# Optimization experiments

Hardware: AMD Instinct MI355X
Metric: run time of the kernel (lower is better)

## Reference

```python
import jax, jax.numpy as jnp
import numpy as np

NEG = -9.0e15

def gat_layer(X, adj_mask, W, Wb, a1, a2, ab):
    # X: [N, Fin]; W: [Fin, Fout]; a1,a2: [Fout]; ab: scalar
    h = X @ W + Wb                                   # [N, Fout]
    # a([h_i || h_j]) = h_i@a1 + h_j@a2 + ab  (decomposition of concat+linear)
    e = jax.nn.leaky_relu((h @ a1)[:, None] + (h @ a2)[None, :] + ab,
                          negative_slope=0.2)        # [N, N]
    e = jnp.where(adj_mask, e, NEG)
    attn = jax.nn.softmax(e, axis=1)                 # [N, N]
    return jax.nn.elu(attn @ h)                      # [N, Fout]

def setup_inputs() -> dict:
    key = jax.random.key(0)
    ks = jax.random.split(key, 12)
    N, Fin, Fh, H, Fout = 4096, 512, 128, 4, 64
    X = jax.random.normal(ks[0], (N, Fin), dtype=jnp.float32)
    adjacency_matrix = jax.random.randint(ks[1], (N, N), 0, 2, dtype=jnp.int32)
    s_in = 1.0 / np.sqrt(Fin)
    s_a = 1.0 / np.sqrt(2 * Fh)
    W_h  = jax.random.uniform(ks[2], (H, Fin, Fh), jnp.float32, -s_in, s_in)
    b_h  = jax.random.uniform(ks[3], (H, Fh), jnp.float32, -s_in, s_in)
    a1_h = jax.random.uniform(ks[4], (H, Fh), jnp.float32, -s_a, s_a)
    a2_h = jax.random.uniform(ks[5], (H, Fh), jnp.float32, -s_a, s_a)
    ab_h = jax.random.uniform(ks[6], (H,), jnp.float32, -s_a, s_a)
    Fcat = H * Fh
    s_c = 1.0 / np.sqrt(Fcat)
    s_ao = 1.0 / np.sqrt(2 * Fout)
    W_o  = jax.random.uniform(ks[7], (Fcat, Fout), jnp.float32, -s_c, s_c)
    b_o  = jax.random.uniform(ks[8], (Fout,), jnp.float32, -s_c, s_c)
    a1_o = jax.random.uniform(ks[9], (Fout,), jnp.float32, -s_ao, s_ao)
    a2_o = jax.random.uniform(ks[10], (Fout,), jnp.float32, -s_ao, s_ao)
    ab_o = jax.random.uniform(ks[11], (), jnp.float32, -s_ao, s_ao)
    return {"X": X, "adjacency_matrix": adjacency_matrix,
            "W_h": W_h, "b_h": b_h, "a1_h": a1_h, "a2_h": a2_h, "ab_h": ab_h,
            "W_o": W_o, "b_o": b_o, "a1_o": a1_o, "a2_o": a2_o, "ab_o": ab_o}

def reference(X, adjacency_matrix, W_h, b_h, a1_h, a2_h, ab_h,
              W_o, b_o, a1_o, a2_o, ab_o):
    adj_mask = adjacency_matrix > 0
    # per-head attention layers, vmapped over heads
    heads = jax.vmap(gat_layer, in_axes=(None, None, 0, 0, 0, 0, 0))(
        X, adj_mask, W_h, b_h, a1_h, a2_h, ab_h)      # [H, N, Fh]
    H, N, Fh = heads.shape
    x = jnp.transpose(heads, (1, 0, 2)).reshape(N, H * Fh)  # concat along features
    x = gat_layer(x, adj_mask, W_o, b_o, a1_o, a2_o, ab_o)  # [N, Fout]
    return jax.nn.log_softmax(x, axis=1)
```

## Files before the change

### kernel.cpp

```cpp
#include <hip/hip_runtime.h>
#include <math.h>

#define NN 4096
#define LOG2E 1.44269504088896340736f

using f32x2  = __attribute__((ext_vector_type(2))) float;
using f32x4  = __attribute__((ext_vector_type(4))) float;
using bf16x4 = __attribute__((ext_vector_type(4))) __bf16;
using bf16x8 = __attribute__((ext_vector_type(8))) __bf16;

#if __has_builtin(__builtin_amdgcn_exp2f)
#define EXP2(x) __builtin_amdgcn_exp2f(x)
#else
#define EXP2(x) __expf((x) * 0.6931471805599453f)
#endif

__device__ __forceinline__ void barrier_lgkm() {
    asm volatile("s_waitcnt lgkmcnt(0)\ns_barrier" ::: "memory");
}

template<int FH>
__device__ __forceinline__ void stage_tile(const __bf16* __restrict__ hgp,
                                           __bf16* dst, int tid) {
#pragma unroll
    for (int it = 0; it < FH / 32; it++) {
        int c = tid + it * 256;
        int f = c >> 3, sl = c & 7;
        int g = sl ^ (f & 7);
        __builtin_amdgcn_global_load_lds(
            (const __attribute__((address_space(1))) void*)(hgp + (size_t)f * NN + g * 8),
            (__attribute__((address_space(3))) void*)(dst + (size_t)c * 8), 16, 0, 0);
    }
}

__device__ __forceinline__ void stage_g(const __bf16* __restrict__ base, int ldk,
                                        __bf16* dst, int tid) {
#pragma unroll
    for (int it = 0; it < 2; it++) {
        int c = tid + it * 256;
        int f = c >> 3, sl = c & 7;
        int g = sl ^ (f & 7);
        __builtin_amdgcn_global_load_lds(
            (const __attribute__((address_space(1))) void*)(base + (size_t)f * ldk + g * 8),
            (__attribute__((address_space(3))) void*)(dst + (size_t)c * 8), 16, 0, 0);
    }
}

__global__ void pack_adj_kernel(const int* __restrict__ adj,
                                unsigned long long* __restrict__ bits) {
    int gw = (blockIdx.x * blockDim.x + threadIdx.x) >> 6;
    int lane = threadIdx.x & 63;
    int v = adj[(size_t)gw * 64 + lane];
    unsigned long long m = __ballot(v > 0);
    if (lane == 0) bits[gw] = m;
}

__global__ void prepack_kernel(const float* __restrict__ W_h, const float* __restrict__ b_h,
                               const float* __restrict__ W_o,
                               __bf16* __restrict__ Bt1, float* __restrict__ biasp,
                               __bf16* __restrict__ Bt2) {
    int idx = blockIdx.x * 256 + threadIdx.x;
    {
        int n = idx >> 9, k = idx & 511;
        int h = n >> 7, f = n & 127;
        Bt1[idx] = (__bf16)W_h[(size_t)h * 512 * 128 + k * 128 + f];
    }
    if (idx < 64 * 512) {
        int n = idx >> 9, k = idx & 511;
        Bt2[idx] = (__bf16)W_o[k * 64 + n];
    }
    if (idx < 512) biasp[idx] = b_h[idx];
}

__global__ void cast_bf16_kernel(const float* __restrict__ src, __bf16* __restrict__ dst) {
    int i = blockIdx.x * 256 + threadIdx.x;
    f32x4 v = *(const f32x4*)(src + (size_t)i * 4);
    bf16x4 o;
#pragma unroll
    for (int q = 0; q < 4; q++) o[q] = (__bf16)v[q];
    *(bf16x4*)(dst + (size_t)i * 4) = o;
}

__global__ __launch_bounds__(256) void gemm_fused_kernel(
    const __bf16* __restrict__ A, const __bf16* __restrict__ Bt,
    const float* __restrict__ bias,
    const float* __restrict__ a1, const float* __restrict__ a2,
    __bf16* __restrict__ Ht, float* __restrict__ s1, float* __restrict__ s2,
    int M, int N, int K)
{
    __shared__ __attribute__((aligned(16))) __bf16 As[2][64 * 64];
    __shared__ __attribute__((aligned(16))) __bf16 Bs[2][64 * 64];
    const int tid = threadIdx.x, w = tid >> 6, l = tid & 63, o = l >> 4, rl = l & 15;
    const int bm = blockIdx.y * 64, bn = blockIdx.x * 64;
    f32x4 acc[4] = {};
    stage_g(A + (size_t)bm * K, K, &As[0][0], tid);
    stage_g(Bt + (size_t)bn * K, K, &Bs[0][0], tid);
    const int KB = K / 64;
    for (int kb = 0; kb < KB; kb++) {
        int b = kb & 1;
        __syncthreads();
        if (kb + 1 < KB) {
            stage_g(A + (size_t)bm * K + (kb + 1) * 64, K, &As[b ^ 1][0], tid);
            stage_g(Bt + (size_t)bn * K + (kb + 1) * 64, K, &Bs[b ^ 1][0], tid);
        }
#pragma unroll
        for (int kt = 0; kt < 2; kt++) {
            int ra = w * 16 + rl;
            int cg = kt * 4 + o;
            bf16x8 af = *(const bf16x8*)(&As[b][(ra * 8 + (cg ^ (ra & 7))) * 8]);
#pragma unroll
            for (int nt = 0; nt < 4; nt++) {
                int rb = nt * 16 + rl;
                bf16x8 bfr = *(const bf16x8*)(&Bs[b][(rb * 8 + (cg ^ (rb & 7))) * 8]);
                acc[nt] = __builtin_amdgcn_mfma_f32_16x16x32_bf16(af, bfr, acc[nt], 0, 0, 0);
            }
        }
    }
    const int head = bn >> 7;
    const int row_base = bm + w * 16 + o * 4;
    float p1[4] = {0.f, 0.f, 0.f, 0.f}, p2[4] = {0.f, 0.f, 0.f, 0.f};
#pragma unroll
    for (int nt = 0; nt < 4; nt++) {
        int col = bn + nt * 16 + rl;
        float bv = bias[col];
        float a1v = a1[col] * LOG2E, a2v = a2[col] * LOG2E;
        bf16x4 hv;
#pragma unroll
        for (int r4 = 0; r4 < 4; r4++) {
            float h = acc[nt][r4] + bv;
            hv[r4] = (__bf16)h;
            p1[r4] += h * a1v;
            p2[r4] += h * a2v;
        }
        *(bf16x4*)(Ht + (size_t)col * M + row_base) = hv;
    }
#pragma unroll
    for (int r4 = 0; r4 < 4; r4++)
#pragma unroll
        for (int off = 1; off < 16; off <<= 1) {
            p1[r4] += __shfl_xor(p1[r4], off, 64);
            p2[r4] += __shfl_xor(p2[r4], off, 64);
        }
    if (rl == 0)
#pragma unroll
        for (int r4 = 0; r4 < 4; r4++) {
            atomicAdd(&s1[(size_t)head * M + row_base + r4], p1[r4]);
            atomicAdd(&s2[(size_t)head * M + row_base + r4], p2[r4]);
        }
}

__global__ void smax_kernel(const float* __restrict__ s2, float* __restrict__ s2max) {
    const float* p = s2 + (size_t)blockIdx.x * NN;
    int t = threadIdx.x;
    float m = -INFINITY;
    for (int i = t; i < NN; i += 256) m = fmaxf(m, p[i]);
#pragma unroll
    for (int off = 1; off < 64; off <<= 1) m = fmaxf(m, __shfl_xor(m, off, 64));
    __shared__ float red[4];
    if ((t & 63) == 0) red[t >> 6] = m;
    __syncthreads();
    if (t == 0) s2max[blockIdx.x] = fmaxf(fmaxf(red[0], red[1]), fmaxf(red[2], red[3]));
}

template<int FH, int JSPLIT>
__global__ __launch_bounds__(256, 4) void attn_kernel(
    const __bf16* __restrict__ Htg,
    const unsigned long long* __restrict__ adj_bits,
    const float* __restrict__ s1_all, const float* __restrict__ s2_all,
    const float* __restrict__ s2max_all, const float* __restrict__ ab_all,
    __bf16* __restrict__ accp,
    float* __restrict__ lg,
    int ldo)
{
    constexpr int NJT = NN / 64 / JSPLIT;
    constexpr int NTW = FH / 64;
    const int head = blockIdx.y;
    const int js   = blockIdx.z;
    const int row0 = blockIdx.x * 64;
    const int jt0  = js * NJT;
    const int tid = threadIdx.x;
    const int w = tid >> 6, l = tid & 63, o = l >> 4, rl = l & 15;
    const int myrow = row0 + w * 16 + rl;

    __shared__ __attribute__((aligned(16))) __bf16 hbuf[2][FH * 64];
    __shared__ __attribute__((aligned(16))) __bf16 plds[8 * 64 * 8];

    const float* s2 = s2_all + (size_t)head * NN;
    const __bf16* hg = Htg + (size_t)head * FH * NN;
    const float s1r = s1_all[(size_t)head * NN + myrow] + ab_all[head] * LOG2E;
    float mrow; { float x = s1r + s2max_all[head]; mrow = fmaxf(x, 0.2f * x); }
    const float u0 = s1r - mrow;
    const float v0 = fmaf(0.2f, s1r, -mrow);
    float lacc = 0.f;
    f32x4 acc[4][NTW] = {};

    unsigned long long aw;
    f32x4 sA0, sB0, sA1, sB1;
    bf16x8 fc0, fc1;
    bf16x8 fn0, fn1;

    auto PLOAD = [&](int jt) {
        aw = adj_bits[(size_t)myrow * 64 + jt];
        const float* sp = s2 + jt * 64 + o * 8;
        sA0 = *(const f32x4*)(sp);       sB0 = *(const f32x4*)(sp + 4);
        sA1 = *(const f32x4*)(sp + 32);  sB1 = *(const f32x4*)(sp + 36);
    };
    auto PMATH = [&](bf16x8& f0, bf16x8& f1) {
        float ps = 0.f;
        {
            unsigned int mb = (unsigned int)(aw >> (o * 8)) & 0xFFu;
#pragma unroll
            for (int q = 0; q < 8; q++) {
                float s = (q < 4) ? sA0[q] : sB0[q - 4];
                float t = fmaxf(s + u0, fmaf(0.2f, s, v0));
                t = ((mb >> q) & 1u) ? t : -1.0e20f;
                float p = EXP2(t);
                f0[q] = (__bf16)p; ps += p;
            }
        }
        {
            unsigned int mb = (unsigned int)(aw >> (32 + o * 8)) & 0xFFu;
#pragma unroll
            for (int q = 0; q < 8; q++) {
                float s = (q < 4) ? sA1[q] : sB1[q - 4];
                float t = fmaxf(s + u0, fmaf(0.2f, s, v0));
                t = ((mb >> q) & 1u) ? t : -1.0e20f;
                float p = EXP2(t);
                f1[q] = (__bf16)p; ps += p;
            }
        }
        lacc += ps;
    };

    stage_tile<FH>(hg + (size_t)jt0 * 64, &hbuf[0][0], tid);
    PLOAD(jt0);
    PMATH(fc0, fc1);
    PLOAD(jt0 + 1);

    for (int jl = 0; jl < NJT; jl++) {
        const int b = jl & 1;
        const int jt = jt0 + jl;
        *(bf16x8*)(&plds[((w * 2 + 0) * 64 + l) * 8]) = fc0;
        *(bf16x8*)(&plds[((w * 2 + 1) * 64 + l) * 8]) = fc1;
        __syncthreads();
        if (jl + 1 < NJT) {
            stage_tile<FH>(hg + (size_t)(jt + 1) * 64, &hbuf[b ^ 1][0], tid);
            PMATH(fn0, fn1);
        }
        if (jl + 2 < NJT) PLOAD(jt + 2);
        __builtin_amdgcn_s_setprio(1);
#pragma unroll
        for (int kt = 0; kt < 2; kt++) {
            bf16x8 b0, b1;
            {
                int f = (w * NTW + 0) * 16 + rl;
                int slot = (kt * 4 + o) ^ (rl & 7);
                b0 = *(const bf16x8*)(&hbuf[b][(f * 8 + slot) * 8]);
            }
            if constexpr (NTW > 1) {
                int f = (w * NTW + 1) * 16 + rl;
                int slot = (kt * 4 + o) ^ (rl & 7);
                b1 = *(const bf16x8*)(&hbuf[b][(f * 8 + slot) * 8]);
            }
#pragma unroll
            for (int mt = 0; mt < 4; mt++) {
                bf16x8 af = (mt == w) ? (kt ? fc1 : fc0)
                          : *(const bf16x8*)(&plds[((mt * 2 + kt) * 64 + l) * 8]);
                acc[mt][0] = __builtin_amdgcn_mfma_f32_16x16x32_bf16(
                    af, b0, acc[mt][0], 0, 0, 0);
                if constexpr (NTW > 1)
                    acc[mt][1] = __builtin_amdgcn_mfma_f32_16x16x32_bf16(
                        af, b1, acc[mt][1], 0, 0, 0);
            }
        }
        __builtin_amdgcn_s_setprio(0);
        barrier_lgkm();
        fc0 = fn0; fc1 = fn1;
    }
    lacc += __shfl_xor(lacc, 16, 64);
    lacc += __shfl_xor(lacc, 32, 64);
    if (l < 16) lg[((size_t)head * JSPLIT + js) * NN + row0 + w * 16 + l] = lacc;
#pragma unroll
    for (int mt = 0; mt < 4; mt++)
#pragma unroll
        for (int ntl = 0; ntl < NTW; ntl++)
#pragma unroll
            for (int r4 = 0; r4 < 4; r4++) {
                int grow = row0 + mt * 16 + o * 4 + r4;
                int gcol = head * FH + (w * NTW + ntl) * 16 + rl;
                accp[((size_t)js * NN + grow) * ldo + gcol] = (__bf16)acc[mt][ntl][r4];
            }
}

__global__ void combine1_kernel(const __bf16* __restrict__ accp, const float* __restrict__ lg,
                                __bf16* __restrict__ outb) {
    int gid = blockIdx.x * 256 + threadIdx.x;
    int row = gid >> 7, c4 = (gid & 127) * 4;
    int head = c4 >> 7;
    float lsum = 0.f;
#pragma unroll
    for (int js = 0; js < 4; js++) lsum += lg[((size_t)head * 4 + js) * NN + row];
    float inv = lsum > 0.f ? 1.f / lsum : 0.f;
    float v[4] = {0.f, 0.f, 0.f, 0.f};
#pragma unroll
    for (int js = 0; js < 4; js++) {
        bf16x4 t = *(const bf16x4*)(accp + ((size_t)js * NN + row) * 512 + c4);
#pragma unroll
        for (int q = 0; q < 4; q++) v[q] += (float)t[q];
    }
    bf16x4 ob;
#pragma unroll
    for (int q = 0; q < 4; q++) {
        float x = v[q] * inv;
        x = x > 0.f ? x : __expf(x) - 1.f;
        ob[q] = (__bf16)x;
    }
    *(bf16x4*)(outb + (size_t)row * 512 + c4) = ob;
}

__global__ void combine2_kernel(const __bf16* __restrict__ accp, const float* __restrict__ lg,
                                float* __restrict__ out) {
    int row = (blockIdx.x * 256 + threadIdx.x) >> 6;
    int lane = threadIdx.x & 63;
    if (row >= NN) return;
    float lsum = 0.f, v = 0.f;
#pragma unroll
    for (int js = 0; js < 16; js++) {
        lsum += lg[(size_t)js * NN + row];
        v += (float)accp[((size_t)js * NN + row) * 64 + lane];
    }
    float inv = lsum > 0.f ? 1.f / lsum : 0.f;
    v *= inv;
    v = v > 0.f ? v : __expf(v) - 1.f;
    float m = v;
#pragma unroll
    for (int off = 1; off < 64; off <<= 1) m = fmaxf(m, __shfl_xor(m, off, 64));
    float ex = __expf(v - m);
    float s = ex;
#pragma unroll
    for (int off = 1; off < 64; off <<= 1) s += __shfl_xor(s, off, 64);
    out[(size_t)row * 64 + lane] = v - m - __logf(s);
}

extern "C" void kernel_launch(void* const* d_in, const int* in_sizes, int n_in,
                              void* d_out, int out_size, void* d_ws, size_t ws_size,
                              hipStream_t stream) {
    const float* X    = (const float*)d_in[0];
    const int*   adj  = (const int*)d_in[1];
    const float* W_h  = (const float*)d_in[2];
    const float* b_h  = (const float*)d_in[3];
    const float* a1_h = (const float*)d_in[4];
    const float* a2_h = (const float*)d_in[5];
    const float* ab_h = (const float*)d_in[6];
    const float* W_o  = (const float*)d_in[7];
    const float* b_o  = (const float*)d_in[8];
    const float* a1_o = (const float*)d_in[9];
    const float* a2_o = (const float*)d_in[10];
    const float* ab_o = (const float*)d_in[11];
    float* out = (float*)d_out;

    char* ws = (char*)d_ws;
    auto alloc = [&](size_t bytes) {
        char* p = ws; ws += (bytes + 255) & ~(size_t)255; return p;
    };
    unsigned long long* adj_bits = (unsigned long long*)alloc((size_t)NN * 64 * 8);
    __bf16* Bt1    = (__bf16*)alloc((size_t)512 * 512 * 2);
    float*  biasp  = (float*)alloc(512 * 4);
    __bf16* Bt2    = (__bf16*)alloc((size_t)64 * 512 * 2);
    __bf16* Xb     = (__bf16*)alloc((size_t)NN * 512 * 2);
    float*  s1h    = (float*)alloc((size_t)4 * NN * 4);
    float*  s2h    = (float*)alloc((size_t)4 * NN * 4);
    float*  s1o    = (float*)alloc((size_t)NN * 4);
    float*  s2o    = (float*)alloc((size_t)NN * 4);
    float*  s2maxh = (float*)alloc(4 * 4);
    float*  s2maxo = (float*)alloc(4);
    __bf16* Htg    = (__bf16*)alloc((size_t)512 * NN * 2);
    __bf16* accp1  = (__bf16*)alloc((size_t)4 * NN * 512 * 2);
    float*  lg1    = (float*)alloc((size_t)16 * NN * 4);
    __bf16* outhb  = (__bf16*)alloc((size_t)NN * 512 * 2);
    __bf16* Ht2    = (__bf16*)alloc((size_t)64 * NN * 2);
    __bf16* accp2  = (__bf16*)alloc((size_t)16 * NN * 64 * 2);
    float*  lg2    = (float*)alloc((size_t)16 * NN * 4);

    hipMemsetAsync(s1h, 0, (size_t)(4 + 4 + 1 + 1) * NN * 4, stream);
    pack_adj_kernel<<<(NN * 64) / 4, 256, 0, stream>>>(adj, adj_bits);
    prepack_kernel<<<1024, 256, 0, stream>>>(W_h, b_h, W_o, Bt1, biasp, Bt2);
    cast_bf16_kernel<<<(NN * 512 / 4) / 256, 256, 0, stream>>>(X, Xb);
    gemm_fused_kernel<<<dim3(8, 64), 256, 0, stream>>>(
        Xb, Bt1, biasp, a1_h, a2_h, Htg, s1h, s2h, NN, 512, 512);
    smax_kernel<<<4, 256, 0, stream>>>(s2h, s2maxh);
    attn_kernel<128, 4><<<dim3(NN / 64, 4, 4), 256, 0, stream>>>(
        Htg, adj_bits, s1h, s2h, s2maxh, ab_h, accp1, lg1, 512);
    combine1_kernel<<<(NN * 128) / 256, 256, 0, stream>>>(accp1, lg1, outhb);
    gemm_fused_kernel<<<dim3(1, 64), 256, 0, stream>>>(
        outhb, Bt2, b_o, a1_o, a2_o, Ht2, s1o, s2o, NN, 64, 512);
    smax_kernel<<<1, 256, 0, stream>>>(s2o, s2maxo);
    attn_kernel<64, 16><<<dim3(NN / 64, 1, 16), 256, 0, stream>>>(
        Ht2, adj_bits, s1o, s2o, s2maxo, ab_o, accp2, lg2, 64);
    combine2_kernel<<<(NN * 64) / 256, 256, 0, stream>>>(accp2, lg2, out);
}
```

Before: 227.0 us.

## Give each wave its own row block, dropping the P exchange through LDS

The attention kernel now has each wave multiply its own 16-row probability fragment against the full FH-wide value tile, instead of sharing P fragments across waves through an LDS buffer. This removes the plds store and reads and the trailing barrier in each tile iteration, and frees that LDS. In exchange, each wave reads the whole value tile from LDS, several times more B-operand traffic per wave. The software pipelining that computed the next tile's probabilities ahead of time is also gone, so the exp math now sits on the critical path just before the MFMAs.

```diff
diff --git a/kernel.cpp b/kernel.cpp
--- a/kernel.cpp
+++ b/kernel.cpp
@@ -14,10 +14,6 @@
 #else
 #define EXP2(x) __expf((x) * 0.6931471805599453f)
 #endif
-
-__device__ __forceinline__ void barrier_lgkm() {
-    asm volatile("s_waitcnt lgkmcnt(0)\ns_barrier" ::: "memory");
-}
 
 template<int FH>
 __device__ __forceinline__ void stage_tile(const __bf16* __restrict__ hgp,
@@ -173,7 +169,7 @@
     int ldo)
 {
     constexpr int NJT = NN / 64 / JSPLIT;
-    constexpr int NTW = FH / 64;
+    constexpr int NTL = FH / 16;
     const int head = blockIdx.y;
     const int js   = blockIdx.z;
     const int row0 = blockIdx.x * 64;
@@ -183,7 +179,6 @@
     const int myrow = row0 + w * 16 + rl;
 
     __shared__ __attribute__((aligned(16))) __bf16 hbuf[2][FH * 64];
-    __shared__ __attribute__((aligned(16))) __bf16 plds[8 * 64 * 8];
 
     const float* s2 = s2_all + (size_t)head * NN;
     const __bf16* hg = Htg + (size_t)head * FH * NN;
@@ -192,12 +187,10 @@
     const float u0 = s1r - mrow;
     const float v0 = fmaf(0.2f, s1r, -mrow);
     float lacc = 0.f;
-    f32x4 acc[4][NTW] = {};
+    f32x4 acc[NTL] = {};
 
     unsigned long long aw;
     f32x4 sA0, sB0, sA1, sB1;
-    bf16x8 fc0, fc1;
-    bf16x8 fn0, fn1;
 
     auto PLOAD = [&](int jt) {
         aw = adj_bits[(size_t)myrow * 64 + jt];
@@ -234,62 +227,40 @@
 
     stage_tile<FH>(hg + (size_t)jt0 * 64, &hbuf[0][0], tid);
     PLOAD(jt0);
-    PMATH(fc0, fc1);
-    PLOAD(jt0 + 1);
 
     for (int jl = 0; jl < NJT; jl++) {
         const int b = jl & 1;
         const int jt = jt0 + jl;
-        *(bf16x8*)(&plds[((w * 2 + 0) * 64 + l) * 8]) = fc0;
-        *(bf16x8*)(&plds[((w * 2 + 1) * 64 + l) * 8]) = fc1;
         __syncthreads();
-        if (jl + 1 < NJT) {
+        if (jl + 1 < NJT)
             stage_tile<FH>(hg + (size_t)(jt + 1) * 64, &hbuf[b ^ 1][0], tid);
-            PMATH(fn0, fn1);
-        }
-        if (jl + 2 < NJT) PLOAD(jt + 2);
+        bf16x8 fc0, fc1;
+        PMATH(fc0, fc1);
+        if (jl + 1 < NJT) PLOAD(jt + 1);
         __builtin_amdgcn_s_setprio(1);
 #pragma unroll
-        for (int kt = 0; kt < 2; kt++) {
-            bf16x8 b0, b1;
-            {
-                int f = (w * NTW + 0) * 16 + rl;
-                int slot = (kt * 4 + o) ^ (rl & 7);
-                b0 = *(const bf16x8*)(&hbuf[b][(f * 8 + slot) * 8]);
-            }
-            if constexpr (NTW > 1) {
-                int f = (w * NTW + 1) * 16 + rl;
-                int slot = (kt * 4 + o) ^ (rl & 7);
-                b1 = *(const bf16x8*)(&hbuf[b][(f * 8 + slot) * 8]);
-            }
-#pragma unroll
-            for (int mt = 0; mt < 4; mt++) {
-                bf16x8 af = (mt == w) ? (kt ? fc1 : fc0)
-                          : *(const bf16x8*)(&plds[((mt * 2 + kt) * 64 + l) * 8]);
-                acc[mt][0] = __builtin_amdgcn_mfma_f32_16x16x32_bf16(
-                    af, b0, acc[mt][0], 0, 0, 0);
-                if constexpr (NTW > 1)
-                    acc[mt][1] = __builtin_amdgcn_mfma_f32_16x16x32_bf16(
-                        af, b1, acc[mt][1], 0, 0, 0);
-            }
+        for (int ntl = 0; ntl < NTL; ntl++) {
+            int f = ntl * 16 + rl;
+            int s0 = o ^ (rl & 7);
+            int s1 = (4 + o) ^ (rl & 7);
+            bf16x8 b0 = *(const bf16x8*)(&hbuf[b][(f * 8 + s0) * 8]);
+            bf16x8 b1 = *(const bf16x8*)(&hbuf[b][(f * 8 + s1) * 8]);
+            acc[ntl] = __builtin_amdgcn_mfma_f32_16x16x32_bf16(fc0, b0, acc[ntl], 0, 0, 0);
+            acc[ntl] = __builtin_amdgcn_mfma_f32_16x16x32_bf16(fc1, b1, acc[ntl], 0, 0, 0);
         }
         __builtin_amdgcn_s_setprio(0);
-        barrier_lgkm();
-        fc0 = fn0; fc1 = fn1;
     }
     lacc += __shfl_xor(lacc, 16, 64);
     lacc += __shfl_xor(lacc, 32, 64);
     if (l < 16) lg[((size_t)head * JSPLIT + js) * NN + row0 + w * 16 + l] = lacc;
 #pragma unroll
-    for (int mt = 0; mt < 4; mt++)
-#pragma unroll
-        for (int ntl = 0; ntl < NTW; ntl++)
-#pragma unroll
-            for (int r4 = 0; r4 < 4; r4++) {
-                int grow = row0 + mt * 16 + o * 4 + r4;
-                int gcol = head * FH + (w * NTW + ntl) * 16 + rl;
-                accp[((size_t)js * NN + grow) * ldo + gcol] = (__bf16)acc[mt][ntl][r4];
-            }
+    for (int ntl = 0; ntl < NTL; ntl++)
+#pragma unroll
+        for (int r4 = 0; r4 < 4; r4++) {
+            int grow = row0 + w * 16 + o * 4 + r4;
+            int gcol = head * FH + ntl * 16 + rl;
+            accp[((size_t)js * NN + grow) * ldo + gcol] = (__bf16)acc[ntl][r4];
+        }
 }
 
 __global__ void combine1_kernel(const __bf16* __restrict__ accp, const float* __restrict__ lg,
```

Result: faster. 219.0 us (-3.5%).
